# Optimization experiments

Measured on AMD Instinct MI355X. Metric: run time of the kernel, lower is better.

The kernel has to match this reference:

```python
import jax, jax.numpy as jnp
import numpy as np

N = 100000
E = 3200000
NFEAT, NHID, NCLASS = 512, 256, 64
K = 10
ALPHA = 0.1


def setup_inputs() -> dict:
    key = jax.random.key(0)
    k1, k2, k3, k4, k5 = jax.random.split(key, 5)
    x = jax.random.normal(k1, (N, NFEAT), dtype=jnp.float32)
    edge_index = jax.random.randint(k2, (2, E), 0, N, dtype=jnp.int64)
    # Linear params (Kaiming-ish scale)
    W1 = jax.random.normal(k3, (NFEAT, NHID), dtype=jnp.float32) / np.sqrt(NFEAT)
    b1 = jnp.zeros((NHID,), dtype=jnp.float32)
    W2 = jax.random.normal(k4, (NHID, NCLASS), dtype=jnp.float32) / np.sqrt(NHID)
    b2 = jnp.zeros((NCLASS,), dtype=jnp.float32)
    # GPR coefficients: temp[k] = alpha*(1-alpha)^k, temp[K] = (1-alpha)^K
    temp = ALPHA * (1.0 - ALPHA) ** np.arange(K + 1)
    temp[-1] = (1.0 - ALPHA) ** K
    temp = jnp.asarray(temp, dtype=jnp.float32)
    return {"x": x, "edge_index": edge_index, "W1": W1, "b1": b1,
            "W2": W2, "b2": b2, "temp": temp}


def _gcn_norm(edge_index, num_nodes):
    # add self-loops, symmetric GCN normalization (PyG gcn_norm, edge_weight=1)
    loop = jnp.arange(num_nodes, dtype=edge_index.dtype)
    src = jnp.concatenate([edge_index[0], loop])
    dst = jnp.concatenate([edge_index[1], loop])
    deg = jnp.zeros((num_nodes,), dtype=jnp.float32).at[dst].add(1.0)
    dinv = jnp.where(deg > 0, jax.lax.rsqrt(deg), 0.0)
    norm = dinv[src] * dinv[dst]
    return src, dst, norm


def reference(x, edge_index, W1, b1, W2, b2, temp):
    n = x.shape[0]
    # eval mode: dropout is identity
    h = jax.nn.relu(x @ W1 + b1)
    h = h @ W2 + b2  # [N, nclass]
    src, dst, norm = _gcn_norm(edge_index, n)
    hidden = h * temp[0]
    for k in range(K):
        # one GCN-normalized hop: out[dst] += norm * h[src]
        h = jax.ops.segment_sum(norm[:, None] * h[src], dst, num_segments=n)
        hidden = hidden + temp[k + 1] * h
    return jax.nn.log_softmax(hidden, axis=1)
```

## Files before the change

kernel.cpp:

```cpp
#include <hip/hip_runtime.h>

#define N_NODES 100000
#define N_EDGES 3200000
#define NFEAT 512
#define NHID 256
#define NCLASS 64
#define KHOPS 10
#define SCAN_B 391

#define NBSHIFT 9
#define NBUCK 196
#define BCAP 20480
#define TILE 4096

typedef __bf16 bf16x8 __attribute__((ext_vector_type(8)));
typedef __bf16 bf16x4 __attribute__((ext_vector_type(4)));
typedef float f32x4 __attribute__((ext_vector_type(4)));


__global__ __launch_bounds__(256) void zero_deg_kernel(int* __restrict__ deg, int* __restrict__ bcursor) {
    int i = blockIdx.x * 256 + threadIdx.x;
    if (i < N_NODES) deg[i] = 0;
    if (blockIdx.x == 0 && threadIdx.x < NBUCK) bcursor[threadIdx.x] = 0;
}

__global__ __launch_bounds__(256) void deg_kernel(const int* __restrict__ ei, int* __restrict__ deg) {
    int e = blockIdx.x * 256 + threadIdx.x;
    if (e < N_EDGES) atomicAdd(&deg[ei[N_EDGES + e]], 1);
}

__global__ __launch_bounds__(256) void dinv_kernel(const int* __restrict__ deg, float* __restrict__ dinv) {
    int i = blockIdx.x * 256 + threadIdx.x;
    if (i < N_NODES) dinv[i] = rsqrtf((float)(deg[i] + 1));
}


__global__ __launch_bounds__(256) void radix1_kernel(const int* __restrict__ ei,
                                                     int* __restrict__ bcursor,
                                                     int2* __restrict__ breg) {
    __shared__ int2 stage[TILE];
    __shared__ int hist[NBUCK];
    __shared__ int base[NBUCK];
    __shared__ int offs[NBUCK];
    int t = threadIdx.x;
    int e0 = blockIdx.x * TILE;
    int n = N_EDGES - e0; if (n > TILE) n = TILE;
    for (int i = t; i < NBUCK; i += 256) { hist[i] = 0; offs[i] = 0; }
    __syncthreads();
    for (int i = t; i < n; i += 256) {
        int s = ei[e0 + i];
        int d = ei[N_EDGES + e0 + i];
        stage[i] = make_int2(s, d);
        atomicAdd(&hist[d >> NBSHIFT], 1);
    }
    __syncthreads();
    for (int i = t; i < NBUCK; i += 256)
        if (hist[i]) base[i] = atomicAdd(&bcursor[i], hist[i]);
    __syncthreads();
    for (int i = t; i < n; i += 256) {
        int2 e = stage[i];
        int b = e.y >> NBSHIFT;
        int slot = base[b] + atomicAdd(&offs[b], 1);
        if (slot < BCAP) breg[(size_t)b * BCAP + slot] = e;
    }
}


__global__ __launch_bounds__(256) void bucket_deg_kernel(const int2* __restrict__ breg,
                                                         const int* __restrict__ bcursor,
                                                         int* __restrict__ deg,
                                                         float* __restrict__ dinv) {
    __shared__ int cnt[512];
    int b = blockIdx.x;
    int t = threadIdx.x;
    cnt[t] = 0; cnt[t + 256] = 0;
    __syncthreads();
    int n = bcursor[b]; if (n > BCAP) n = BCAP;
    const int2* bp = breg + (size_t)b * BCAP;
    for (int i = t; i < n; i += 256)
        atomicAdd(&cnt[bp[i].y & 511], 1);
    __syncthreads();
    int d0 = b << NBSHIFT;
    for (int j = t; j < 512; j += 256) {
        int i = d0 + j;
        if (i < N_NODES) {
            int d = cnt[j];
            deg[i] = d;
            dinv[i] = rsqrtf((float)(d + 1));
        }
    }
}


__global__ __launch_bounds__(256) void scan1_kernel(const int* __restrict__ deg, int* __restrict__ partial) {
    __shared__ int red[256];
    int t = threadIdx.x;
    int i = blockIdx.x * 256 + t;
    red[t] = (i < N_NODES) ? deg[i] + 1 : 0;
    __syncthreads();
    for (int off = 128; off > 0; off >>= 1) {
        if (t < off) red[t] += red[t + off];
        __syncthreads();
    }
    if (t == 0) partial[blockIdx.x] = red[0];
}

__global__ __launch_bounds__(512) void scan2_kernel(int* __restrict__ partial) {
    __shared__ int s[512];
    int t = threadIdx.x;
    int v = (t < SCAN_B) ? partial[t] : 0;
    s[t] = v;
    __syncthreads();
    for (int off = 1; off < 512; off <<= 1) {
        int add = (t >= off) ? s[t - off] : 0;
        __syncthreads();
        s[t] += add;
        __syncthreads();
    }
    if (t < SCAN_B) partial[t] = s[t] - v;
}

__global__ __launch_bounds__(256) void scan3_kernel(const int* __restrict__ deg,
                                                    const int* __restrict__ partial,
                                                    int* __restrict__ row_ptr,
                                                    int* __restrict__ cursor) {
    __shared__ int s[256];
    int t = threadIdx.x;
    int i = blockIdx.x * 256 + t;
    int v = (i < N_NODES) ? deg[i] + 1 : 0;
    s[t] = v;
    __syncthreads();
    for (int off = 1; off < 256; off <<= 1) {
        int add = (t >= off) ? s[t - off] : 0;
        __syncthreads();
        s[t] += add;
        __syncthreads();
    }
    int excl = s[t] - v + partial[blockIdx.x];
    if (i < N_NODES) {
        row_ptr[i] = excl;
        cursor[i] = excl;
        if (i == N_NODES - 1) row_ptr[N_NODES] = excl + v;
    }
}


__global__ __launch_bounds__(256) void radix2_kernel(const int2* __restrict__ breg,
                                                     const int* __restrict__ bcursor,
                                                     const int* __restrict__ row_ptr,
                                                     int* __restrict__ esrc) {
    __shared__ int lcur[512];
    int b = blockIdx.x;
    int t = threadIdx.x;
    int d0 = b << NBSHIFT;
    int nn = N_NODES - d0; if (nn > 512) nn = 512;
    for (int j = t; j < nn; j += 256) {
        int rp = row_ptr[d0 + j];
        lcur[j] = rp + 1;
        esrc[rp] = d0 + j;
    }
    __syncthreads();
    int cnt = bcursor[b]; if (cnt > BCAP) cnt = BCAP;
    const int2* bp = breg + (size_t)b * BCAP;
    for (int i = t; i < cnt; i += 256) {
        int2 e = bp[i];
        int p = atomicAdd(&lcur[e.y - d0], 1);
        esrc[p] = e.x;
    }
}

__global__ __launch_bounds__(256) void fill_kernel(const int* __restrict__ ei,
                                                   int* __restrict__ cursor,
                                                   int* __restrict__ esrc) {
    int e = blockIdx.x * 256 + threadIdx.x;
    if (e < N_EDGES) {
        int s = ei[e], d = ei[N_EDGES + e];
        int p = atomicAdd(&cursor[d], 1);
        esrc[p] = s;
    } else if (e < N_EDGES + N_NODES) {
        int i = e - N_EDGES;
        int p = atomicAdd(&cursor[i], 1);
        esrc[p] = i;
    }
}


__global__ __launch_bounds__(256) void wprep_kernel(const float* __restrict__ W1,
                                                    const float* __restrict__ W2,
                                                    __bf16* __restrict__ w1t,
                                                    __bf16* __restrict__ w2t) {
    int i = blockIdx.x * 256 + threadIdx.x;
    if (i < NFEAT * NHID) {
        int n = i >> 9, k = i & 511;
        w1t[i] = (__bf16)W1[k * NHID + n];
    } else {
        int j = i - NFEAT * NHID;
        if (j < NHID * NCLASS) {
            int n = j >> 8, k = j & 255;
            w2t[j] = (__bf16)W2[k * NCLASS + n];
        }
    }
}


#define MT 128
#define KC 64
#define XP 72
#define WP 72
#define HP 264

__global__ __launch_bounds__(512, 4) void mlp_kernel(const float* __restrict__ x,
                                                     const __bf16* __restrict__ w1t,
                                                     const float* __restrict__ b1,
                                                     const __bf16* __restrict__ w2t,
                                                     const float* __restrict__ b2,
                                                     const float* __restrict__ dinv,
                                                     __bf16* __restrict__ u0) {
    __shared__ char smem[67584] __attribute__((aligned(16)));
    __bf16* xs  = (__bf16*)smem;
    __bf16* wt  = (__bf16*)(smem + 18432);
    __bf16* h1s = (__bf16*)smem;

    int t = threadIdx.x;
    int wv = t >> 6, lane = t & 63;
    int lrow = lane & 15;
    int quad = lane >> 4;
    int row0 = blockIdx.x * MT;
    int wm = (wv >> 2) * 64;
    int wn = (wv & 3) * 64;

    const float* xpt[2];
    int xr[2], xc8[2];
    #pragma unroll
    for (int it = 0; it < 2; ++it) {
        int j = it * 512 + t;
        int r = j >> 3, c8 = j & 7;
        int rr = row0 + r; if (rr >= N_NODES) rr = N_NODES - 1;
        xpt[it] = &x[(size_t)rr * NFEAT + c8 * 8];
        xr[it] = r; xc8[it] = c8;
    }
    float4 px[4];
    px[0] = *(const float4*)(xpt[0]);
    px[1] = *(const float4*)(xpt[0] + 4);
    px[2] = *(const float4*)(xpt[1]);
    px[3] = *(const float4*)(xpt[1] + 4);

    f32x4 acc[4][4] = {};
    #pragma unroll 1
    for (int kc = 0; kc < NFEAT; kc += KC) {
        __syncthreads();
        #pragma unroll
        for (int it = 0; it < 2; ++it) {
            float4 v0 = px[it * 2], v1 = px[it * 2 + 1];
            bf16x8 o = { (__bf16)v0.x, (__bf16)v0.y, (__bf16)v0.z, (__bf16)v0.w,
                         (__bf16)v1.x, (__bf16)v1.y, (__bf16)v1.z, (__bf16)v1.w };
            *(bf16x8*)&xs[xr[it] * XP + xc8[it] * 8] = o;
        }
        #pragma unroll
        for (int it = 0; it < 4; ++it) {
            int j = it * 512 + t;
            int n = j >> 3, c8 = j & 7;
            *(bf16x8*)&wt[n * WP + c8 * 8] = *(const bf16x8*)&w1t[(size_t)n * NFEAT + kc + c8 * 8];
        }
        __syncthreads();
        if (kc + KC < NFEAT) {
            px[0] = *(const float4*)(xpt[0] + kc + KC);
            px[1] = *(const float4*)(xpt[0] + kc + KC + 4);
            px[2] = *(const float4*)(xpt[1] + kc + KC);
            px[3] = *(const float4*)(xpt[1] + kc + KC + 4);
        }
        #pragma unroll
        for (int ks = 0; ks < 2; ++ks) {
            int kof = ks * 32 + quad * 8;
            bf16x8 a[4], b[4];
            #pragma unroll
            for (int mt = 0; mt < 4; ++mt)
                a[mt] = *(const bf16x8*)&xs[(wm + mt * 16 + lrow) * XP + kof];
            #pragma unroll
            for (int nt = 0; nt < 4; ++nt)
                b[nt] = *(const bf16x8*)&wt[(wn + nt * 16 + lrow) * WP + kof];
            #pragma unroll
            for (int mt = 0; mt < 4; ++mt)
                #pragma unroll
                for (int nt = 0; nt < 4; ++nt)
                    acc[mt][nt] = __builtin_amdgcn_mfma_f32_16x16x32_bf16(a[mt], b[nt], acc[mt][nt], 0, 0, 0);
        }
    }
    __syncthreads();
    #pragma unroll
    for (int nt = 0; nt < 4; ++nt) {
        int coln = wn + nt * 16 + lrow;
        float bb = b1[coln];
        #pragma unroll
        for (int mt = 0; mt < 4; ++mt) {
            int rbase = wm + mt * 16 + quad * 4;
            #pragma unroll
            for (int r = 0; r < 4; ++r) {
                float v = acc[mt][nt][r] + bb;
                h1s[(rbase + r) * HP + coln] = (__bf16)fmaxf(v, 0.f);
            }
        }
    }
    __syncthreads();
    int rg = (wv >> 1) * 32;
    int cg = (wv & 1) * 32;
    f32x4 acc2[2][2] = {};
    #pragma unroll
    for (int ks = 0; ks < 8; ++ks) {
        int kof = ks * 32 + quad * 8;
        bf16x8 a2[2], bv[2];
        #pragma unroll
        for (int m2 = 0; m2 < 2; ++m2)
            a2[m2] = *(const bf16x8*)&h1s[(rg + m2 * 16 + lrow) * HP + kof];
        #pragma unroll
        for (int nt = 0; nt < 2; ++nt)
            bv[nt] = *(const bf16x8*)&w2t[(size_t)(cg + nt * 16 + lrow) * NHID + kof];
        #pragma unroll
        for (int m2 = 0; m2 < 2; ++m2)
            #pragma unroll
            for (int nt = 0; nt < 2; ++nt)
                acc2[m2][nt] = __builtin_amdgcn_mfma_f32_16x16x32_bf16(a2[m2], bv[nt], acc2[m2][nt], 0, 0, 0);
    }
    #pragma unroll
    for (int m2 = 0; m2 < 2; ++m2) {
        #pragma unroll
        for (int nt = 0; nt < 2; ++nt) {
            int coln = cg + nt * 16 + lrow;
            float bb = b2[coln];
            #pragma unroll
            for (int r = 0; r < 4; ++r) {
                int row = row0 + rg + m2 * 16 + quad * 4 + r;
                if (row < N_NODES) {
                    float v = acc2[m2][nt][r] + bb;
                    u0[(size_t)row * NCLASS + coln] = (__bf16)(dinv[row] * v);
                }
            }
        }
    }
}


__global__ __launch_bounds__(256) void prop_kernel(const __bf16* __restrict__ uin,
                                                   __bf16* __restrict__ uout,
                                                   const int* __restrict__ row_ptr,
                                                   const int* __restrict__ esrc,
                                                   const float* __restrict__ dinv) {
    int node = blockIdx.x * 4 + (threadIdx.x >> 6);
    int lane = threadIdx.x & 63;
    int oct = lane >> 3, fi8 = lane & 7;
    int beg = row_ptr[node], end = row_ptr[node + 1];
    const uint4* urow = (const uint4*)uin;
    float acc[8] = {};
    int nit = (end - beg + 7) >> 3;
    #pragma unroll 4
    for (int it = 0; it < nit; ++it) {
        int e = beg + it * 8 + oct;
        int ec = min(e, end - 1);
        int s = __builtin_nontemporal_load(&esrc[ec]);
        float m = (e < end) ? 1.f : 0.f;
        uint4 v = urow[(size_t)s * 8 + fi8];
        unsigned vv;
        vv = v.x;
        acc[0] = fmaf(m, __int_as_float(vv << 16), acc[0]);
        acc[1] = fmaf(m, __int_as_float(vv & 0xffff0000u), acc[1]);
        vv = v.y;
        acc[2] = fmaf(m, __int_as_float(vv << 16), acc[2]);
        acc[3] = fmaf(m, __int_as_float(vv & 0xffff0000u), acc[3]);
        vv = v.z;
        acc[4] = fmaf(m, __int_as_float(vv << 16), acc[4]);
        acc[5] = fmaf(m, __int_as_float(vv & 0xffff0000u), acc[5]);
        vv = v.w;
        acc[6] = fmaf(m, __int_as_float(vv << 16), acc[6]);
        acc[7] = fmaf(m, __int_as_float(vv & 0xffff0000u), acc[7]);
    }
    #pragma unroll
    for (int j = 0; j < 8; ++j) {
        acc[j] += __shfl_xor(acc[j], 8);
        acc[j] += __shfl_xor(acc[j], 16);
        acc[j] += __shfl_xor(acc[j], 32);
    }
    if (oct == 0) {
        float di = dinv[node];
        float d2 = di * di;
        union { __bf16 b[8]; uint4 u; } pk;
        #pragma unroll
        for (int j = 0; j < 8; ++j) pk.b[j] = (__bf16)(d2 * acc[j]);
        ((uint4*)uout)[(size_t)node * 8 + fi8] = pk.u;
    }
}


__global__ __launch_bounds__(256) void finale_kernel(const __bf16* __restrict__ ubuf,
                                                     const float* __restrict__ dinv,
                                                     const float* __restrict__ temp,
                                                     float* __restrict__ out) {
    int node = blockIdx.x * 4 + (threadIdx.x >> 6);
    int j = threadIdx.x & 63;
    const unsigned short* ub = (const unsigned short*)ubuf;
    float acc = 0.f;
    #pragma unroll
    for (int k = 0; k <= KHOPS; ++k) {
        unsigned short us = __builtin_nontemporal_load(
            &ub[(size_t)k * N_NODES * NCLASS + (size_t)node * NCLASS + j]);
        acc = fmaf(temp[k], __int_as_float((unsigned)us << 16), acc);
    }
    float v = acc / dinv[node];
    float m = v;
    #pragma unroll
    for (int o = 32; o > 0; o >>= 1) m = fmaxf(m, __shfl_xor(m, o));
    float ex = expf(v - m);
    float s = ex;
    #pragma unroll
    for (int o = 32; o > 0; o >>= 1) s += __shfl_xor(s, o);
    out[(size_t)node * 64 + j] = v - m - logf(s);
}

extern "C" void kernel_launch(void* const* d_in, const int* in_sizes, int n_in,
                              void* d_out, int out_size, void* d_ws, size_t ws_size,
                              hipStream_t stream) {
    const float* x    = (const float*)d_in[0];
    const int*   ei   = (const int*)d_in[1];
    const float* W1   = (const float*)d_in[2];
    const float* b1   = (const float*)d_in[3];
    const float* W2   = (const float*)d_in[4];
    const float* b2   = (const float*)d_in[5];
    const float* temp = (const float*)d_in[6];
    float* out = (float*)d_out;

    char* ws = (char*)d_ws;
    size_t off = 0;
    auto alloc = [&](size_t bytes) -> void* {
        void* p = ws + off;
        off = (off + bytes + 255) & ~(size_t)255;
        return p;
    };
    int*    deg     = (int*)alloc((size_t)N_NODES * 4);
    float*  dinv    = (float*)alloc((size_t)N_NODES * 4);
    int*    row_ptr = (int*)alloc((size_t)(N_NODES + 1) * 4);
    int*    cursor  = (int*)alloc((size_t)N_NODES * 4);
    int*    partial = (int*)alloc((size_t)SCAN_B * 4);
    int*    bcursor = (int*)alloc((size_t)NBUCK * 4);
    int*    esrc    = (int*)alloc((size_t)(N_EDGES + N_NODES) * 4);
    __bf16* ubuf    = (__bf16*)alloc((size_t)(KHOPS + 1) * N_NODES * NCLASS * 2);
    __bf16* w1t     = (__bf16*)alloc((size_t)NFEAT * NHID * 2);
    __bf16* w2t     = (__bf16*)alloc((size_t)NHID * NCLASS * 2);
    size_t breg_bytes = (size_t)NBUCK * BCAP * 8;
    bool use_radix = (off + breg_bytes <= ws_size);
    int2* breg = use_radix ? (int2*)alloc(breg_bytes) : (int2*)0;

    zero_deg_kernel<<<(N_NODES + 255) / 256, 256, 0, stream>>>(deg, bcursor);
    if (use_radix) {
        radix1_kernel<<<(N_EDGES + TILE - 1) / TILE, 256, 0, stream>>>(ei, bcursor, breg);
        bucket_deg_kernel<<<NBUCK, 256, 0, stream>>>(breg, bcursor, deg, dinv);
        scan1_kernel<<<SCAN_B, 256, 0, stream>>>(deg, partial);
        scan2_kernel<<<1, 512, 0, stream>>>(partial);
        scan3_kernel<<<SCAN_B, 256, 0, stream>>>(deg, partial, row_ptr, cursor);
        radix2_kernel<<<NBUCK, 256, 0, stream>>>(breg, bcursor, row_ptr, esrc);
    } else {
        deg_kernel<<<(N_EDGES + 255) / 256, 256, 0, stream>>>(ei, deg);
        dinv_kernel<<<(N_NODES + 255) / 256, 256, 0, stream>>>(deg, dinv);
        scan1_kernel<<<SCAN_B, 256, 0, stream>>>(deg, partial);
        scan2_kernel<<<1, 512, 0, stream>>>(partial);
        scan3_kernel<<<SCAN_B, 256, 0, stream>>>(deg, partial, row_ptr, cursor);
        fill_kernel<<<(N_EDGES + N_NODES + 255) / 256, 256, 0, stream>>>(ei, cursor, esrc);
    }
    wprep_kernel<<<(NFEAT * NHID + NHID * NCLASS + 255) / 256, 256, 0, stream>>>(W1, W2, w1t, w2t);

    mlp_kernel<<<(N_NODES + MT - 1) / MT, 512, 0, stream>>>(x, w1t, b1, w2t, b2, dinv, ubuf);

    const size_t ustride = (size_t)N_NODES * NCLASS;
    for (int k = 0; k < KHOPS; ++k) {
        prop_kernel<<<N_NODES / 4, 256, 0, stream>>>(ubuf + (size_t)k * ustride,
                                                     ubuf + (size_t)(k + 1) * ustride,
                                                     row_ptr, esrc, dinv);
    }

    finale_kernel<<<N_NODES / 4, 256, 0, stream>>>(ubuf, dinv, temp, out);
}
```

Before: 995.1 us.

## Split features into 16-wide slices so propagation gathers fit in L2

Stores the propagated node features in four separate 16-column slice buffers and runs all ten propagation hops per slice. Each slice's node table is a quarter the size of the full table, so the random neighbour gathers are meant to hit in L2 cache more often. In exchange, the CSR edge list is re-read four times as often, each gather moves only 32 bytes per edge, and the number of kernel launches quadruples. The MLP output and the final combine kernel are changed to use the sliced layout.

```diff
diff --git a/kernel.cpp b/kernel.cpp
--- a/kernel.cpp
+++ b/kernel.cpp
@@ -12,6 +12,9 @@
 #define NBUCK 196
 #define BCAP 20480
 #define TILE 4096
+
+#define SW 16
+#define NSL 4
 
 typedef __bf16 bf16x8 __attribute__((ext_vector_type(8)));
 typedef __bf16 bf16x4 __attribute__((ext_vector_type(4)));
@@ -321,18 +324,20 @@
             for (int nt = 0; nt < 2; ++nt)
                 acc2[m2][nt] = __builtin_amdgcn_mfma_f32_16x16x32_bf16(a2[m2], bv[nt], acc2[m2][nt], 0, 0, 0);
     }
+    const size_t sls = (size_t)(KHOPS + 1) * N_NODES * SW;
     #pragma unroll
     for (int m2 = 0; m2 < 2; ++m2) {
         #pragma unroll
         for (int nt = 0; nt < 2; ++nt) {
             int coln = cg + nt * 16 + lrow;
             float bb = b2[coln];
+            int sl = coln >> 4, cin = coln & 15;
             #pragma unroll
             for (int r = 0; r < 4; ++r) {
                 int row = row0 + rg + m2 * 16 + quad * 4 + r;
                 if (row < N_NODES) {
                     float v = acc2[m2][nt][r] + bb;
-                    u0[(size_t)row * NCLASS + coln] = (__bf16)(dinv[row] * v);
+                    u0[(size_t)sl * sls + (size_t)row * SW + cin] = (__bf16)(dinv[row] * v);
                 }
             }
         }
@@ -347,45 +352,38 @@
                                                    const float* __restrict__ dinv) {
     int node = blockIdx.x * 4 + (threadIdx.x >> 6);
     int lane = threadIdx.x & 63;
-    int oct = lane >> 3, fi8 = lane & 7;
+    int eslot = lane >> 2, q = lane & 3;
     int beg = row_ptr[node], end = row_ptr[node + 1];
-    const uint4* urow = (const uint4*)uin;
-    float acc[8] = {};
-    int nit = (end - beg + 7) >> 3;
-    #pragma unroll 4
+    const unsigned long long* ub = (const unsigned long long*)uin;
+    float acc[4] = {};
+    int nit = (end - beg + 15) >> 4;
+    #pragma unroll 2
     for (int it = 0; it < nit; ++it) {
-        int e = beg + it * 8 + oct;
+        int e = beg + it * 16 + eslot;
         int ec = min(e, end - 1);
         int s = __builtin_nontemporal_load(&esrc[ec]);
         float m = (e < end) ? 1.f : 0.f;
-        uint4 v = urow[(size_t)s * 8 + fi8];
-        unsigned vv;
-        vv = v.x;
-        acc[0] = fmaf(m, __int_as_float(vv << 16), acc[0]);
-        acc[1] = fmaf(m, __int_as_float(vv & 0xffff0000u), acc[1]);
-        vv = v.y;
-        acc[2] = fmaf(m, __int_as_float(vv << 16), acc[2]);
-        acc[3] = fmaf(m, __int_as_float(vv & 0xffff0000u), acc[3]);
-        vv = v.z;
-        acc[4] = fmaf(m, __int_as_float(vv << 16), acc[4]);
-        acc[5] = fmaf(m, __int_as_float(vv & 0xffff0000u), acc[5]);
-        vv = v.w;
-        acc[6] = fmaf(m, __int_as_float(vv << 16), acc[6]);
-        acc[7] = fmaf(m, __int_as_float(vv & 0xffff0000u), acc[7]);
-    }
-    #pragma unroll
-    for (int j = 0; j < 8; ++j) {
+        unsigned long long v = ub[(size_t)s * 4 + q];
+        unsigned lo = (unsigned)v, hi = (unsigned)(v >> 32);
+        acc[0] = fmaf(m, __int_as_float(lo << 16), acc[0]);
+        acc[1] = fmaf(m, __int_as_float(lo & 0xffff0000u), acc[1]);
+        acc[2] = fmaf(m, __int_as_float(hi << 16), acc[2]);
+        acc[3] = fmaf(m, __int_as_float(hi & 0xffff0000u), acc[3]);
+    }
+    #pragma unroll
+    for (int j = 0; j < 4; ++j) {
+        acc[j] += __shfl_xor(acc[j], 4);
         acc[j] += __shfl_xor(acc[j], 8);
         acc[j] += __shfl_xor(acc[j], 16);
         acc[j] += __shfl_xor(acc[j], 32);
     }
-    if (oct == 0) {
+    if (eslot == 0) {
         float di = dinv[node];
         float d2 = di * di;
-        union { __bf16 b[8]; uint4 u; } pk;
-        #pragma unroll
-        for (int j = 0; j < 8; ++j) pk.b[j] = (__bf16)(d2 * acc[j]);
-        ((uint4*)uout)[(size_t)node * 8 + fi8] = pk.u;
+        union { __bf16 b[4]; unsigned long long u; } pk;
+        #pragma unroll
+        for (int j = 0; j < 4; ++j) pk.b[j] = (__bf16)(d2 * acc[j]);
+        __builtin_nontemporal_store(pk.u, &((unsigned long long*)uout)[(size_t)node * 4 + q]);
     }
 }
 
@@ -396,12 +394,13 @@
                                                      float* __restrict__ out) {
     int node = blockIdx.x * 4 + (threadIdx.x >> 6);
     int j = threadIdx.x & 63;
-    const unsigned short* ub = (const unsigned short*)ubuf;
+    int sl = j >> 4, cin = j & 15;
+    const unsigned short* ub = (const unsigned short*)ubuf
+        + (size_t)sl * (KHOPS + 1) * N_NODES * SW + (size_t)node * SW + cin;
     float acc = 0.f;
     #pragma unroll
     for (int k = 0; k <= KHOPS; ++k) {
-        unsigned short us = __builtin_nontemporal_load(
-            &ub[(size_t)k * N_NODES * NCLASS + (size_t)node * NCLASS + j]);
+        unsigned short us = __builtin_nontemporal_load(ub + (size_t)k * N_NODES * SW);
         acc = fmaf(temp[k], __int_as_float((unsigned)us << 16), acc);
     }
     float v = acc / dinv[node];
@@ -441,7 +440,7 @@
     int*    partial = (int*)alloc((size_t)SCAN_B * 4);
     int*    bcursor = (int*)alloc((size_t)NBUCK * 4);
     int*    esrc    = (int*)alloc((size_t)(N_EDGES + N_NODES) * 4);
-    __bf16* ubuf    = (__bf16*)alloc((size_t)(KHOPS + 1) * N_NODES * NCLASS * 2);
+    __bf16* ubuf    = (__bf16*)alloc((size_t)NSL * (KHOPS + 1) * N_NODES * SW * 2);
     __bf16* w1t     = (__bf16*)alloc((size_t)NFEAT * NHID * 2);
     __bf16* w2t     = (__bf16*)alloc((size_t)NHID * NCLASS * 2);
     size_t breg_bytes = (size_t)NBUCK * BCAP * 8;
@@ -468,11 +467,14 @@
 
     mlp_kernel<<<(N_NODES + MT - 1) / MT, 512, 0, stream>>>(x, w1t, b1, w2t, b2, dinv, ubuf);
 
-    const size_t ustride = (size_t)N_NODES * NCLASS;
-    for (int k = 0; k < KHOPS; ++k) {
-        prop_kernel<<<N_NODES / 4, 256, 0, stream>>>(ubuf + (size_t)k * ustride,
-                                                     ubuf + (size_t)(k + 1) * ustride,
-                                                     row_ptr, esrc, dinv);
+    const size_t plane = (size_t)N_NODES * SW;
+    const size_t sls   = (size_t)(KHOPS + 1) * plane;
+    for (int s = 0; s < NSL; ++s) {
+        for (int k = 0; k < KHOPS; ++k) {
+            prop_kernel<<<N_NODES / 4, 256, 0, stream>>>(ubuf + (size_t)s * sls + (size_t)k * plane,
+                                                         ubuf + (size_t)s * sls + (size_t)(k + 1) * plane,
+                                                         row_ptr, esrc, dinv);
+        }
     }
 
     finale_kernel<<<N_NODES / 4, 256, 0, stream>>>(ubuf, dinv, temp, out);
```

After: 2.019 ms. 103% more time.
